# Kernel tuning notes

Hardware: AMD Instinct MI355X
Metric: run time of the kernel (lower is better)

The kernel has to match this reference:

```python
import jax, jax.numpy as jnp
import numpy as np

N = 204800  # total nodes in the batched graph
B = 4096    # number of graphs (sessions)
D = 128     # embedding_dim


def setup_inputs() -> dict:
    key = jax.random.key(0)
    ks = jax.random.split(key, 10)
    feat_i = jax.random.normal(ks[0], (N, D), dtype=jnp.float32)
    U_feat = jax.random.normal(ks[1], (B, D), dtype=jnp.float32)
    # per-node click counts >= 1 so log(cnt) is finite
    cnt = jax.random.uniform(ks[2], (N,), dtype=jnp.float32, minval=1.0, maxval=50.0)
    scale = 1.0 / np.sqrt(D)
    W_key = jax.random.normal(ks[3], (D, D), dtype=jnp.float32) * scale
    W_user = jax.random.normal(ks[4], (D, D), dtype=jnp.float32) * scale
    b_user = jax.random.normal(ks[5], (D,), dtype=jnp.float32) * scale
    W_last = jax.random.normal(ks[6], (D, D), dtype=jnp.float32) * scale
    w_e = jax.random.normal(ks[7], (D, 1), dtype=jnp.float32) * scale
    last_nodes = jax.random.randint(ks[8], (B,), 0, N, dtype=jnp.int32)
    segment_ids = jnp.sort(jax.random.randint(ks[9], (N,), 0, B, dtype=jnp.int32))
    return {
        "feat_i": feat_i, "U_feat": U_feat, "cnt": cnt,
        "W_key": W_key, "W_user": W_user, "b_user": b_user,
        "W_last": W_last, "w_e": w_e,
        "last_nodes": last_nodes, "segment_ids": segment_ids,
    }


def reference(feat_i, U_feat, cnt, W_key, W_user, b_user, W_last, w_e,
              last_nodes, segment_ids):
    # linear projections (torch Linear y = x W^T + b; weights here are stored
    # pre-transposed so x @ W is the same math)
    feat_key = feat_i @ W_key                       # [N, D]
    U = U_feat @ W_user + b_user                    # [B, D]
    last_feat = feat_i[last_nodes] @ W_last         # [B, D]
    # dgl.broadcast_nodes: per-graph query replicated onto its nodes
    feat_qry = (U + last_feat)[segment_ids]         # [N, D]
    # additive-sigmoid attention score + log-count bias
    e = jax.nn.sigmoid(feat_qry + feat_key) @ w_e   # [N, 1]
    e = e + jnp.log(cnt)[:, None]                   # [N, 1]
    # segment softmax over ragged per-graph node segments
    m = jax.ops.segment_max(e, segment_ids, num_segments=B)      # [B, 1]
    ex = jnp.exp(e - m[segment_ids])                             # [N, 1]
    s = jax.ops.segment_sum(ex, segment_ids, num_segments=B)     # [B, 1]
    alpha = ex / s[segment_ids]                                  # [N, 1]
    # weighted segment reduce over raw node features (feat_val = feat_i)
    rst = jax.ops.segment_sum(alpha * feat_i, segment_ids, num_segments=B)  # [B, D]
    return rst
```

## Files before the change

### kernel.cpp

```cpp
#include <hip/hip_runtime.h>
#include <hip/hip_bf16.h>
#include <math.h>

#define N_NODES 204800
#define B_GRAPHS 4096
#define DIM 128

typedef __attribute__((ext_vector_type(8))) short bf16x8;
typedef __attribute__((ext_vector_type(4))) float f32x4;

__device__ __forceinline__ float sigf(float x) {
    return 1.0f / (1.0f + __expf(-x));
}

__device__ __forceinline__ unsigned short bfrne(float x) {
    unsigned u = __float_as_uint(x);
    unsigned r = u + 0x7FFFu + ((u >> 16) & 1u);
    return (unsigned short)(r >> 16);
}

__global__ __launch_bounds__(128) void qkernel(
    const float* __restrict__ feat, const float* __restrict__ U_feat,
    const float* __restrict__ W_user, const float* __restrict__ b_user,
    const float* __restrict__ W_last, const int* __restrict__ last_nodes,
    const float* __restrict__ W_key, unsigned short* __restrict__ Wt,
    const int* __restrict__ seg, int* __restrict__ bounds,
    float* __restrict__ q) {
  if (blockIdx.x >= 576) {
    int n = (blockIdx.x - 576) * 128 + threadIdx.x;
    int sc = seg[n];
    int sp = (n == 0) ? -1 : seg[n - 1];
    for (int b = sp + 1; b <= sc; ++b) bounds[b] = (b == 0) ? 0 : n;
    if (n == N_NODES - 1)
      for (int b = sc + 1; b <= B_GRAPHS; ++b) bounds[b] = N_NODES;
    return;
  }
  if (blockIdx.x >= 512) {
    int b = blockIdx.x - 512;
#pragma unroll
    for (int j = 0; j < 2; ++j) {
      int o = b * 256 + j * 128 + threadIdx.x;
      int c = o >> 7, k = o & 127;
      Wt[o] = bfrne(W_key[k * DIM + c]);
    }
    return;
  }
  __shared__ float sU[8][DIM];
  __shared__ float sL[8][DIM];
  const int d = threadIdx.x;
  const int g0 = blockIdx.x * 8;
  for (int g = 0; g < 8; ++g) {
    sU[g][d] = U_feat[(g0 + g) * DIM + d];
    int ln = last_nodes[g0 + g];
    sL[g][d] = feat[ln * DIM + d];
  }
  __syncthreads();
  float acc[8];
#pragma unroll
  for (int g = 0; g < 8; ++g) acc[g] = 0.0f;

  for (int kk = 0; kk < 32; ++kk) {
    float wu[4], wl[4];
#pragma unroll
    for (int j = 0; j < 4; ++j) {
      wu[j] = W_user[(kk * 4 + j) * DIM + d];
      wl[j] = W_last[(kk * 4 + j) * DIM + d];
    }
#pragma unroll
    for (int g = 0; g < 8; ++g) {
      float4 u4 = reinterpret_cast<const float4*>(sU[g])[kk];
      float4 l4 = reinterpret_cast<const float4*>(sL[g])[kk];
      acc[g] += u4.x * wu[0] + u4.y * wu[1] + u4.z * wu[2] + u4.w * wu[3];
      acc[g] += l4.x * wl[0] + l4.y * wl[1] + l4.z * wl[2] + l4.w * wl[3];
    }
  }
  float bu = b_user[d];
  for (int g = 0; g < 8; ++g) q[(g0 + g) * DIM + d] = acc[g] + bu;
}

__global__ __launch_bounds__(512, 4) void ekernel(
    const float* __restrict__ feat, const unsigned short* __restrict__ Wt,
    const float* __restrict__ w_e, const float* __restrict__ cnt,
    const int* __restrict__ seg, const float* __restrict__ q,
    float* __restrict__ e) {
  __shared__ unsigned short sW[128 * DIM];
  __shared__ float sWe[DIM];
  const int tid = threadIdx.x;
  const int base = blockIdx.x * 128;
  const int l = tid & 63, w = tid >> 6;
  const int lr = l & 15, lh = l >> 4;
  const int node = base + w * 16 + lr;

  const int sg = seg[node];
  const float lc = cnt[node];

  const float* rp = feat + (size_t)node * DIM + lh * 8;
  float4 fv[4][2];
#pragma unroll
  for (int ks = 0; ks < 4; ++ks) {
    fv[ks][0] = *reinterpret_cast<const float4*>(rp + ks * 32);
    fv[ks][1] = *reinterpret_cast<const float4*>(rp + ks * 32 + 4);
  }

  const uint4* Wt4 = reinterpret_cast<const uint4*>(Wt);
#pragma unroll
  for (int i = 0; i < 4; ++i) {
    int hw = i * 4096 + tid * 8;
    int row = hw >> 7, k0 = hw & 127;
    uint4 wv = Wt4[i * 512 + tid];
    *reinterpret_cast<uint4*>(&sW[row * DIM + (k0 ^ ((row & 7) << 3))]) = wv;
  }
  if (tid < 32)
    reinterpret_cast<float4*>(sWe)[tid] =
        reinterpret_cast<const float4*>(w_e)[tid];

  const float4* q4p = reinterpret_cast<const float4*>(q);
  float4 qv[4];
#pragma unroll
  for (int c = 0; c < 4; ++c) qv[c] = q4p[(size_t)sg * 32 + c * 4 + lh];

  bf16x8 af[4];
#pragma unroll
  for (int ks = 0; ks < 4; ++ks) {
    union { bf16x8 v; unsigned short u[8]; } a;
    a.u[0] = bfrne(fv[ks][0].x); a.u[1] = bfrne(fv[ks][0].y);
    a.u[2] = bfrne(fv[ks][0].z); a.u[3] = bfrne(fv[ks][0].w);
    a.u[4] = bfrne(fv[ks][1].x); a.u[5] = bfrne(fv[ks][1].y);
    a.u[6] = bfrne(fv[ks][1].z); a.u[7] = bfrne(fv[ks][1].w);
    af[ks] = a.v;
  }

  __syncthreads();

  float4 qv2[4];
#pragma unroll
  for (int c = 0; c < 4; ++c) qv2[c] = q4p[(size_t)sg * 32 + 16 + c * 4 + lh];

  float p = 0.0f;
#pragma unroll
  for (int c = 0; c < 8; ++c) {
    const int row = c * 16 + lr;
    bf16x8 wf[4];
#pragma unroll
    for (int ks = 0; ks < 4; ++ks)
      wf[ks] = *reinterpret_cast<const bf16x8*>(
          &sW[row * DIM + ((ks * 32 + lh * 8) ^ ((row & 7) << 3))]);
    float4 we = *reinterpret_cast<const float4*>(&sWe[c * 16 + lh * 4]);

    f32x4 a0 = f32x4{0.f, 0.f, 0.f, 0.f};
#pragma unroll
    for (int ks = 0; ks < 4; ++ks)
      a0 = __builtin_amdgcn_mfma_f32_16x16x32_bf16(wf[ks], af[ks], a0, 0, 0, 0);

    float4 qc = (c < 4) ? qv[c & 3] : qv2[c & 3];
    p += we.x * sigf(a0[0] + qc.x) + we.y * sigf(a0[1] + qc.y) +
         we.z * sigf(a0[2] + qc.z) + we.w * sigf(a0[3] + qc.w);
  }

  p += __shfl_xor(p, 16, 64);
  p += __shfl_xor(p, 32, 64);
  if (lh == 0) e[node] = p + __logf(lc);
}

__global__ __launch_bounds__(256) void skernel(
    const float* __restrict__ feat, const int* __restrict__ bounds,
    const float* __restrict__ e, float* __restrict__ rst) {
  const int wave = threadIdx.x >> 6;
  const int lane = threadIdx.x & 63;
  const int g = blockIdx.x * 4 + wave;
  const int s0 = bounds[g], s1 = bounds[g + 1];

  if (s1 <= s0) {
    if (lane < 32)
      reinterpret_cast<float4*>(rst)[(size_t)g * 32 + lane] =
          float4{0.f, 0.f, 0.f, 0.f};
    return;
  }

  float ls = 0.0f;
  for (int i = s0 + lane; i < s1; i += 64) ls += __expf(e[i]);
#pragma unroll
  for (int off = 32; off >= 1; off >>= 1) ls += __shfl_xor(ls, off, 64);
  const float inv = 1.0f / ls;

  const int c = lane & 31;
  const int h = lane >> 5;
  float4 acc = float4{0.f, 0.f, 0.f, 0.f};
  const float4* feat4 = reinterpret_cast<const float4*>(feat);
  for (int n = s0 + h; n < s1; n += 2) {
    float pp = __expf(e[n]);
    float4 f = feat4[(size_t)n * 32 + c];
    acc.x += pp * f.x;
    acc.y += pp * f.y;
    acc.z += pp * f.z;
    acc.w += pp * f.w;
  }
  acc.x += __shfl_xor(acc.x, 32, 64);
  acc.y += __shfl_xor(acc.y, 32, 64);
  acc.z += __shfl_xor(acc.z, 32, 64);
  acc.w += __shfl_xor(acc.w, 32, 64);
  if (h == 0) {
    float4 r;
    r.x = acc.x * inv; r.y = acc.y * inv; r.z = acc.z * inv; r.w = acc.w * inv;
    reinterpret_cast<float4*>(rst)[(size_t)g * 32 + c] = r;
  }
}

extern "C" void kernel_launch(void* const* d_in, const int* in_sizes, int n_in,
                              void* d_out, int out_size, void* d_ws,
                              size_t ws_size, hipStream_t stream) {
  const float* feat = (const float*)d_in[0];
  const float* U_feat = (const float*)d_in[1];
  const float* cnt = (const float*)d_in[2];
  const float* W_key = (const float*)d_in[3];
  const float* W_user = (const float*)d_in[4];
  const float* b_user = (const float*)d_in[5];
  const float* W_last = (const float*)d_in[6];
  const float* w_e = (const float*)d_in[7];
  const int* last_nodes = (const int*)d_in[8];
  const int* seg = (const int*)d_in[9];
  float* out = (float*)d_out;

  float* q = (float*)d_ws;
  float* e = q + B_GRAPHS * DIM;
  unsigned short* Wt = (unsigned short*)(e + N_NODES);
  int* bounds = (int*)(Wt + DIM * DIM);

  qkernel<<<512 + 64 + N_NODES / 128, 128, 0, stream>>>(
      feat, U_feat, W_user, b_user, W_last, last_nodes, W_key, Wt, seg, bounds, q);
  ekernel<<<N_NODES / 128, 512, 0, stream>>>(feat, Wt, w_e, cnt, seg, q, e);
  skernel<<<B_GRAPHS / 4, 256, 0, stream>>>(feat, bounds, e, out);
}
```

Baseline: 63.77 us.

## Pre-swizzle W_key into MFMA fragment order and loop blocks over node tiles with prefetch

The W_key transpose step now writes bf16 weights directly in per-lane MFMA fragment order, so the energy kernel copies them linearly into LDS and reads fragments without the XOR swizzle. The energy kernel now uses 256-thread blocks that each process 256 nodes in four iterations, prefetching the next tile's features, segment id and count while computing the current one. This spreads the LDS weight fill over four times as many nodes and overlaps global loads with MFMA work. In exchange the grid has fewer blocks and register pressure goes up from holding two sets of feature registers.

```diff
diff --git a/kernel.cpp b/kernel.cpp
--- a/kernel.cpp
+++ b/kernel.cpp
@@ -23,7 +23,7 @@
     const float* __restrict__ feat, const float* __restrict__ U_feat,
     const float* __restrict__ W_user, const float* __restrict__ b_user,
     const float* __restrict__ W_last, const int* __restrict__ last_nodes,
-    const float* __restrict__ W_key, unsigned short* __restrict__ Wt,
+    const float* __restrict__ W_key, unsigned short* __restrict__ Wf,
     const int* __restrict__ seg, int* __restrict__ bounds,
     float* __restrict__ q) {
   if (blockIdx.x >= 576) {
@@ -38,10 +38,15 @@
   if (blockIdx.x >= 512) {
     int b = blockIdx.x - 512;
 #pragma unroll
-    for (int j = 0; j < 2; ++j) {
-      int o = b * 256 + j * 128 + threadIdx.x;
-      int c = o >> 7, k = o & 127;
-      Wt[o] = bfrne(W_key[k * DIM + c]);
+    for (int jj = 0; jj < 2; ++jj) {
+      int o = b * 256 + jj * 128 + threadIdx.x;
+      int j = o & 7;
+      int l = (o >> 3) & 63;
+      int ks = (o >> 9) & 3;
+      int c = o >> 11;
+      int k = ks * 32 + (l >> 4) * 8 + j;
+      int row = c * 16 + (l & 15);
+      Wf[o] = bfrne(W_key[k * DIM + row]);
     }
     return;
   }
@@ -78,88 +83,107 @@
   for (int g = 0; g < 8; ++g) q[(g0 + g) * DIM + d] = acc[g] + bu;
 }
 
-__global__ __launch_bounds__(512, 4) void ekernel(
-    const float* __restrict__ feat, const unsigned short* __restrict__ Wt,
+__global__ __launch_bounds__(256, 4) void ekernel(
+    const float* __restrict__ feat, const unsigned short* __restrict__ Wf,
     const float* __restrict__ w_e, const float* __restrict__ cnt,
     const int* __restrict__ seg, const float* __restrict__ q,
     float* __restrict__ e) {
-  __shared__ unsigned short sW[128 * DIM];
+  __shared__ unsigned short sWf[128 * DIM];
   __shared__ float sWe[DIM];
   const int tid = threadIdx.x;
-  const int base = blockIdx.x * 128;
+  const int base = blockIdx.x * 256;
   const int l = tid & 63, w = tid >> 6;
   const int lr = l & 15, lh = l >> 4;
-  const int node = base + w * 16 + lr;
-
-  const int sg = seg[node];
-  const float lc = cnt[node];
-
-  const float* rp = feat + (size_t)node * DIM + lh * 8;
-  float4 fv[4][2];
-#pragma unroll
-  for (int ks = 0; ks < 4; ++ks) {
-    fv[ks][0] = *reinterpret_cast<const float4*>(rp + ks * 32);
-    fv[ks][1] = *reinterpret_cast<const float4*>(rp + ks * 32 + 4);
-  }
-
-  const uint4* Wt4 = reinterpret_cast<const uint4*>(Wt);
-#pragma unroll
-  for (int i = 0; i < 4; ++i) {
-    int hw = i * 4096 + tid * 8;
-    int row = hw >> 7, k0 = hw & 127;
-    uint4 wv = Wt4[i * 512 + tid];
-    *reinterpret_cast<uint4*>(&sW[row * DIM + (k0 ^ ((row & 7) << 3))]) = wv;
-  }
+
+  const uint4* Wf4 = reinterpret_cast<const uint4*>(Wf);
+  uint4* sWf4 = reinterpret_cast<uint4*>(sWf);
+#pragma unroll
+  for (int i = 0; i < 8; ++i) sWf4[i * 256 + tid] = Wf4[i * 256 + tid];
   if (tid < 32)
     reinterpret_cast<float4*>(sWe)[tid] =
         reinterpret_cast<const float4*>(w_e)[tid];
 
+  int node = base + w * 16 + lr;
+  int sg = seg[node];
+  float lc = cnt[node];
+  float4 fv[4][2];
+  {
+    const float* rp = feat + (size_t)node * DIM + lh * 8;
+#pragma unroll
+    for (int ks = 0; ks < 4; ++ks) {
+      fv[ks][0] = *reinterpret_cast<const float4*>(rp + ks * 32);
+      fv[ks][1] = *reinterpret_cast<const float4*>(rp + ks * 32 + 4);
+    }
+  }
+
+  __syncthreads();
+
   const float4* q4p = reinterpret_cast<const float4*>(q);
-  float4 qv[4];
-#pragma unroll
-  for (int c = 0; c < 4; ++c) qv[c] = q4p[(size_t)sg * 32 + c * 4 + lh];
-
-  bf16x8 af[4];
-#pragma unroll
-  for (int ks = 0; ks < 4; ++ks) {
-    union { bf16x8 v; unsigned short u[8]; } a;
-    a.u[0] = bfrne(fv[ks][0].x); a.u[1] = bfrne(fv[ks][0].y);
-    a.u[2] = bfrne(fv[ks][0].z); a.u[3] = bfrne(fv[ks][0].w);
-    a.u[4] = bfrne(fv[ks][1].x); a.u[5] = bfrne(fv[ks][1].y);
-    a.u[6] = bfrne(fv[ks][1].z); a.u[7] = bfrne(fv[ks][1].w);
-    af[ks] = a.v;
-  }
-
-  __syncthreads();
-
-  float4 qv2[4];
-#pragma unroll
-  for (int c = 0; c < 4; ++c) qv2[c] = q4p[(size_t)sg * 32 + 16 + c * 4 + lh];
-
-  float p = 0.0f;
-#pragma unroll
-  for (int c = 0; c < 8; ++c) {
-    const int row = c * 16 + lr;
-    bf16x8 wf[4];
-#pragma unroll
-    for (int ks = 0; ks < 4; ++ks)
-      wf[ks] = *reinterpret_cast<const bf16x8*>(
-          &sW[row * DIM + ((ks * 32 + lh * 8) ^ ((row & 7) << 3))]);
-    float4 we = *reinterpret_cast<const float4*>(&sWe[c * 16 + lh * 4]);
-
-    f32x4 a0 = f32x4{0.f, 0.f, 0.f, 0.f};
-#pragma unroll
-    for (int ks = 0; ks < 4; ++ks)
-      a0 = __builtin_amdgcn_mfma_f32_16x16x32_bf16(wf[ks], af[ks], a0, 0, 0, 0);
-
-    float4 qc = (c < 4) ? qv[c & 3] : qv2[c & 3];
-    p += we.x * sigf(a0[0] + qc.x) + we.y * sigf(a0[1] + qc.y) +
-         we.z * sigf(a0[2] + qc.z) + we.w * sigf(a0[3] + qc.w);
-  }
-
-  p += __shfl_xor(p, 16, 64);
-  p += __shfl_xor(p, 32, 64);
-  if (lh == 0) e[node] = p + __logf(lc);
+  const bf16x8* sWfb = reinterpret_cast<const bf16x8*>(sWf);
+
+#pragma unroll
+  for (int t = 0; t < 4; ++t) {
+    int nodeN = 0, sgN = 0;
+    float lcN = 0.0f;
+    if (t < 3) {
+      nodeN = base + ((t + 1) * 4 + w) * 16 + lr;
+      sgN = seg[nodeN];
+      lcN = cnt[nodeN];
+    }
+
+    float4 qvA[4];
+#pragma unroll
+    for (int c = 0; c < 4; ++c) qvA[c] = q4p[(size_t)sg * 32 + c * 4 + lh];
+
+    bf16x8 af[4];
+#pragma unroll
+    for (int ks = 0; ks < 4; ++ks) {
+      union { bf16x8 v; unsigned short u[8]; } a;
+      a.u[0] = bfrne(fv[ks][0].x); a.u[1] = bfrne(fv[ks][0].y);
+      a.u[2] = bfrne(fv[ks][0].z); a.u[3] = bfrne(fv[ks][0].w);
+      a.u[4] = bfrne(fv[ks][1].x); a.u[5] = bfrne(fv[ks][1].y);
+      a.u[6] = bfrne(fv[ks][1].z); a.u[7] = bfrne(fv[ks][1].w);
+      af[ks] = a.v;
+    }
+
+    if (t < 3) {
+      const float* rp = feat + (size_t)nodeN * DIM + lh * 8;
+#pragma unroll
+      for (int ks = 0; ks < 4; ++ks) {
+        fv[ks][0] = *reinterpret_cast<const float4*>(rp + ks * 32);
+        fv[ks][1] = *reinterpret_cast<const float4*>(rp + ks * 32 + 4);
+      }
+    }
+
+    float4 qvB[4];
+#pragma unroll
+    for (int c = 0; c < 4; ++c)
+      qvB[c] = q4p[(size_t)sg * 32 + 16 + c * 4 + lh];
+
+    float p = 0.0f;
+#pragma unroll
+    for (int c = 0; c < 8; ++c) {
+      bf16x8 wf[4];
+#pragma unroll
+      for (int ks = 0; ks < 4; ++ks) wf[ks] = sWfb[(c * 4 + ks) * 64 + l];
+
+      f32x4 a0 = f32x4{0.f, 0.f, 0.f, 0.f};
+#pragma unroll
+      for (int ks = 0; ks < 4; ++ks)
+        a0 = __builtin_amdgcn_mfma_f32_16x16x32_bf16(wf[ks], af[ks], a0, 0, 0, 0);
+
+      float4 we = *reinterpret_cast<const float4*>(&sWe[c * 16 + lh * 4]);
+      float4 qc = (c < 4) ? qvA[c & 3] : qvB[c & 3];
+      p += we.x * sigf(a0[0] + qc.x) + we.y * sigf(a0[1] + qc.y) +
+           we.z * sigf(a0[2] + qc.z) + we.w * sigf(a0[3] + qc.w);
+    }
+
+    p += __shfl_xor(p, 16, 64);
+    p += __shfl_xor(p, 32, 64);
+    if (lh == 0) e[node] = p + __logf(lc);
+
+    node = nodeN; sg = sgN; lc = lcN;
+  }
 }
 
 __global__ __launch_bounds__(256) void skernel(
@@ -223,11 +247,11 @@
 
   float* q = (float*)d_ws;
   float* e = q + B_GRAPHS * DIM;
-  unsigned short* Wt = (unsigned short*)(e + N_NODES);
-  int* bounds = (int*)(Wt + DIM * DIM);
+  unsigned short* Wf = (unsigned short*)(e + N_NODES);
+  int* bounds = (int*)(Wf + DIM * DIM);
 
   qkernel<<<512 + 64 + N_NODES / 128, 128, 0, stream>>>(
-      feat, U_feat, W_user, b_user, W_last, last_nodes, W_key, Wt, seg, bounds, q);
-  ekernel<<<N_NODES / 128, 512, 0, stream>>>(feat, Wt, w_e, cnt, seg, q, e);
+      feat, U_feat, W_user, b_user, W_last, last_nodes, W_key, Wf, seg, bounds, q);
+  ekernel<<<N_NODES / 256, 256, 0, stream>>>(feat, Wf, w_e, cnt, seg, q, e);
   skernel<<<B_GRAPHS / 4, 256, 0, stream>>>(feat, bounds, e, out);
 }
```

Result: slower. 71.43 us (+12.0%).

## Fuse score and segment-softmax reduction into one per-graph kernel

Applied to the files above, without the earlier changes.

Merges the attention-score kernel and the segment reduce kernel into a single kernel with one wave per graph. Each wave walks its graph's nodes in 16-node tiles, computes scores with MFMA, and accumulates exp-weighted features from registers already loaded. This avoids reading feat twice and the round trip through the e buffer. It drops the max subtraction, using cnt*exp(p) directly, which is safe only because the scores are bounded. It also loses the per-node parallelism that spreads ragged segments evenly, and each block still loads the full 32KB weight matrix into LDS.

```diff
diff --git a/kernel.cpp b/kernel.cpp
--- a/kernel.cpp
+++ b/kernel.cpp
@@ -58,7 +58,6 @@
   float acc[8];
 #pragma unroll
   for (int g = 0; g < 8; ++g) acc[g] = 0.0f;
-
   for (int kk = 0; kk < 32; ++kk) {
     float wu[4], wl[4];
 #pragma unroll
@@ -78,131 +77,134 @@
   for (int g = 0; g < 8; ++g) q[(g0 + g) * DIM + d] = acc[g] + bu;
 }
 
-__global__ __launch_bounds__(512, 4) void ekernel(
+__global__ __launch_bounds__(256) void gkernel(
     const float* __restrict__ feat, const unsigned short* __restrict__ Wt,
     const float* __restrict__ w_e, const float* __restrict__ cnt,
-    const int* __restrict__ seg, const float* __restrict__ q,
-    float* __restrict__ e) {
+    const int* __restrict__ bounds, const float* __restrict__ q,
+    float* __restrict__ rst) {
   __shared__ unsigned short sW[128 * DIM];
   __shared__ float sWe[DIM];
   const int tid = threadIdx.x;
-  const int base = blockIdx.x * 128;
   const int l = tid & 63, w = tid >> 6;
   const int lr = l & 15, lh = l >> 4;
-  const int node = base + w * 16 + lr;
-
-  const int sg = seg[node];
-  const float lc = cnt[node];
-
-  const float* rp = feat + (size_t)node * DIM + lh * 8;
-  float4 fv[4][2];
-#pragma unroll
-  for (int ks = 0; ks < 4; ++ks) {
-    fv[ks][0] = *reinterpret_cast<const float4*>(rp + ks * 32);
-    fv[ks][1] = *reinterpret_cast<const float4*>(rp + ks * 32 + 4);
-  }
+  const int g = blockIdx.x * 4 + w;
+
+  const int s0 = bounds[g], s1 = bounds[g + 1];
+  const float4* q4p = reinterpret_cast<const float4*>(q);
+  float4 qv[8];
+#pragma unroll
+  for (int c = 0; c < 8; ++c) qv[c] = q4p[(size_t)g * 32 + c * 4 + lh];
 
   const uint4* Wt4 = reinterpret_cast<const uint4*>(Wt);
 #pragma unroll
-  for (int i = 0; i < 4; ++i) {
-    int hw = i * 4096 + tid * 8;
+  for (int i = 0; i < 8; ++i) {
+    int hw = i * 2048 + tid * 8;
     int row = hw >> 7, k0 = hw & 127;
-    uint4 wv = Wt4[i * 512 + tid];
+    uint4 wv = Wt4[i * 256 + tid];
     *reinterpret_cast<uint4*>(&sW[row * DIM + (k0 ^ ((row & 7) << 3))]) = wv;
   }
   if (tid < 32)
     reinterpret_cast<float4*>(sWe)[tid] =
         reinterpret_cast<const float4*>(w_e)[tid];
 
-  const float4* q4p = reinterpret_cast<const float4*>(q);
-  float4 qv[4];
-#pragma unroll
-  for (int c = 0; c < 4; ++c) qv[c] = q4p[(size_t)sg * 32 + c * 4 + lh];
-
-  bf16x8 af[4];
-#pragma unroll
-  for (int ks = 0; ks < 4; ++ks) {
-    union { bf16x8 v; unsigned short u[8]; } a;
-    a.u[0] = bfrne(fv[ks][0].x); a.u[1] = bfrne(fv[ks][0].y);
-    a.u[2] = bfrne(fv[ks][0].z); a.u[3] = bfrne(fv[ks][0].w);
-    a.u[4] = bfrne(fv[ks][1].x); a.u[5] = bfrne(fv[ks][1].y);
-    a.u[6] = bfrne(fv[ks][1].z); a.u[7] = bfrne(fv[ks][1].w);
-    af[ks] = a.v;
-  }
-
   __syncthreads();
 
-  float4 qv2[4];
-#pragma unroll
-  for (int c = 0; c < 4; ++c) qv2[c] = q4p[(size_t)sg * 32 + 16 + c * 4 + lh];
-
-  float p = 0.0f;
-#pragma unroll
-  for (int c = 0; c < 8; ++c) {
-    const int row = c * 16 + lr;
-    bf16x8 wf[4];
-#pragma unroll
-    for (int ks = 0; ks < 4; ++ks)
-      wf[ks] = *reinterpret_cast<const bf16x8*>(
-          &sW[row * DIM + ((ks * 32 + lh * 8) ^ ((row & 7) << 3))]);
-    float4 we = *reinterpret_cast<const float4*>(&sWe[c * 16 + lh * 4]);
-
-    f32x4 a0 = f32x4{0.f, 0.f, 0.f, 0.f};
-#pragma unroll
-    for (int ks = 0; ks < 4; ++ks)
-      a0 = __builtin_amdgcn_mfma_f32_16x16x32_bf16(wf[ks], af[ks], a0, 0, 0, 0);
-
-    float4 qc = (c < 4) ? qv[c & 3] : qv2[c & 3];
-    p += we.x * sigf(a0[0] + qc.x) + we.y * sigf(a0[1] + qc.y) +
-         we.z * sigf(a0[2] + qc.z) + we.w * sigf(a0[3] + qc.w);
-  }
-
-  p += __shfl_xor(p, 16, 64);
-  p += __shfl_xor(p, 32, 64);
-  if (lh == 0) e[node] = p + __logf(lc);
-}
-
-__global__ __launch_bounds__(256) void skernel(
-    const float* __restrict__ feat, const int* __restrict__ bounds,
-    const float* __restrict__ e, float* __restrict__ rst) {
-  const int wave = threadIdx.x >> 6;
-  const int lane = threadIdx.x & 63;
-  const int g = blockIdx.x * 4 + wave;
-  const int s0 = bounds[g], s1 = bounds[g + 1];
-
   if (s1 <= s0) {
-    if (lane < 32)
-      reinterpret_cast<float4*>(rst)[(size_t)g * 32 + lane] =
+    if (l < 32)
+      reinterpret_cast<float4*>(rst)[(size_t)g * 32 + l] =
           float4{0.f, 0.f, 0.f, 0.f};
     return;
   }
 
-  float ls = 0.0f;
-  for (int i = s0 + lane; i < s1; i += 64) ls += __expf(e[i]);
-#pragma unroll
-  for (int off = 32; off >= 1; off >>= 1) ls += __shfl_xor(ls, off, 64);
-  const float inv = 1.0f / ls;
-
-  const int c = lane & 31;
-  const int h = lane >> 5;
-  float4 acc = float4{0.f, 0.f, 0.f, 0.f};
-  const float4* feat4 = reinterpret_cast<const float4*>(feat);
-  for (int n = s0 + h; n < s1; n += 2) {
-    float pp = __expf(e[n]);
-    float4 f = feat4[(size_t)n * 32 + c];
-    acc.x += pp * f.x;
-    acc.y += pp * f.y;
-    acc.z += pp * f.z;
-    acc.w += pp * f.w;
-  }
-  acc.x += __shfl_xor(acc.x, 32, 64);
-  acc.y += __shfl_xor(acc.y, 32, 64);
-  acc.z += __shfl_xor(acc.z, 32, 64);
-  acc.w += __shfl_xor(acc.w, 32, 64);
-  if (h == 0) {
-    float4 r;
-    r.x = acc.x * inv; r.y = acc.y * inv; r.z = acc.z * inv; r.w = acc.w * inv;
-    reinterpret_cast<float4*>(rst)[(size_t)g * 32 + c] = r;
+  float4 acc[4][2];
+#pragma unroll
+  for (int ks = 0; ks < 4; ++ks) {
+    acc[ks][0] = float4{0.f, 0.f, 0.f, 0.f};
+    acc[ks][1] = float4{0.f, 0.f, 0.f, 0.f};
+  }
+  float s = 0.0f;
+
+  const int ntiles = (s1 - s0 + 15) >> 4;
+  for (int t = 0; t < ntiles; ++t) {
+    const int node = s0 + t * 16 + lr;
+    const bool valid = node < s1;
+    const int nc = valid ? node : (s1 - 1);
+
+    const float* rp = feat + (size_t)nc * DIM + lh * 8;
+    float4 fv[4][2];
+#pragma unroll
+    for (int ks = 0; ks < 4; ++ks) {
+      fv[ks][0] = *reinterpret_cast<const float4*>(rp + ks * 32);
+      fv[ks][1] = *reinterpret_cast<const float4*>(rp + ks * 32 + 4);
+    }
+    const float lc = cnt[nc];
+
+    bf16x8 af[4];
+#pragma unroll
+    for (int ks = 0; ks < 4; ++ks) {
+      union { bf16x8 v; unsigned short u[8]; } a;
+      a.u[0] = bfrne(fv[ks][0].x); a.u[1] = bfrne(fv[ks][0].y);
+      a.u[2] = bfrne(fv[ks][0].z); a.u[3] = bfrne(fv[ks][0].w);
+      a.u[4] = bfrne(fv[ks][1].x); a.u[5] = bfrne(fv[ks][1].y);
+      a.u[6] = bfrne(fv[ks][1].z); a.u[7] = bfrne(fv[ks][1].w);
+      af[ks] = a.v;
+    }
+
+    float p = 0.0f;
+#pragma unroll
+    for (int c = 0; c < 8; ++c) {
+      const int row = c * 16 + lr;
+      bf16x8 wf[4];
+#pragma unroll
+      for (int ks = 0; ks < 4; ++ks)
+        wf[ks] = *reinterpret_cast<const bf16x8*>(
+            &sW[row * DIM + ((ks * 32 + lh * 8) ^ ((row & 7) << 3))]);
+      float4 we = *reinterpret_cast<const float4*>(&sWe[c * 16 + lh * 4]);
+
+      f32x4 a0 = f32x4{0.f, 0.f, 0.f, 0.f};
+#pragma unroll
+      for (int ks = 0; ks < 4; ++ks)
+        a0 = __builtin_amdgcn_mfma_f32_16x16x32_bf16(wf[ks], af[ks], a0, 0, 0, 0);
+
+      float4 qc = qv[c];
+      p += we.x * sigf(a0[0] + qc.x) + we.y * sigf(a0[1] + qc.y) +
+           we.z * sigf(a0[2] + qc.z) + we.w * sigf(a0[3] + qc.w);
+    }
+    p += __shfl_xor(p, 16, 64);
+    p += __shfl_xor(p, 32, 64);
+
+    const float wt = valid ? lc * __expf(p) : 0.0f;
+    s += wt;
+#pragma unroll
+    for (int ks = 0; ks < 4; ++ks) {
+      acc[ks][0].x += wt * fv[ks][0].x; acc[ks][0].y += wt * fv[ks][0].y;
+      acc[ks][0].z += wt * fv[ks][0].z; acc[ks][0].w += wt * fv[ks][0].w;
+      acc[ks][1].x += wt * fv[ks][1].x; acc[ks][1].y += wt * fv[ks][1].y;
+      acc[ks][1].z += wt * fv[ks][1].z; acc[ks][1].w += wt * fv[ks][1].w;
+    }
+  }
+
+#pragma unroll
+  for (int m = 1; m <= 8; m <<= 1) {
+    s += __shfl_xor(s, m, 64);
+#pragma unroll
+    for (int ks = 0; ks < 4; ++ks)
+#pragma unroll
+      for (int jh = 0; jh < 2; ++jh) {
+        acc[ks][jh].x += __shfl_xor(acc[ks][jh].x, m, 64);
+        acc[ks][jh].y += __shfl_xor(acc[ks][jh].y, m, 64);
+        acc[ks][jh].z += __shfl_xor(acc[ks][jh].z, m, 64);
+        acc[ks][jh].w += __shfl_xor(acc[ks][jh].w, m, 64);
+      }
+  }
+
+  const float inv = 1.0f / s;
+  if (lr < 8) {
+    const int ks = lr >> 1, jh = lr & 1;
+    float4 v;
+    v.x = acc[ks][jh].x * inv; v.y = acc[ks][jh].y * inv;
+    v.z = acc[ks][jh].z * inv; v.w = acc[ks][jh].w * inv;
+    reinterpret_cast<float4*>(rst)[(size_t)g * 32 + ks * 8 + lh * 2 + jh] = v;
   }
 }
 
@@ -222,12 +224,11 @@
   float* out = (float*)d_out;
 
   float* q = (float*)d_ws;
-  float* e = q + B_GRAPHS * DIM;
-  unsigned short* Wt = (unsigned short*)(e + N_NODES);
+  unsigned short* Wt = (unsigned short*)(q + B_GRAPHS * DIM);
   int* bounds = (int*)(Wt + DIM * DIM);
 
   qkernel<<<512 + 64 + N_NODES / 128, 128, 0, stream>>>(
-      feat, U_feat, W_user, b_user, W_last, last_nodes, W_key, Wt, seg, bounds, q);
-  ekernel<<<N_NODES / 128, 512, 0, stream>>>(feat, Wt, w_e, cnt, seg, q, e);
-  skernel<<<B_GRAPHS / 4, 256, 0, stream>>>(feat, bounds, e, out);
-}
+      feat, U_feat, W_user, b_user, W_last, last_nodes, W_key, Wt, seg,
+      bounds, q);
+  gkernel<<<B_GRAPHS / 4, 256, 0, stream>>>(feat, Wt, w_e, cnt, bounds, q, out);
+}
```

Measured after the change: 75.42 us. 18.3% more time.
